# Performance work log

Measured on AMD Instinct MI355X. Metric: run time of the kernel, lower is better.

## Reference

```python
import jax, jax.numpy as jnp
import numpy as np

EPS = 1e-5   # BatchNorm eps
OUT = 256    # resize target


def _crop_bounds(img):
    # A row/col is 'whitespace' iff all its values are identical (len(unique)==1),
    # i.e. min == max along that axis. This fuses the torch while-loops into reductions.
    col_var = img.min(axis=0) != img.max(axis=0)   # [W] True where column non-constant
    row_var = img.min(axis=1) != img.max(axis=1)   # [H]
    H, W = img.shape
    any_c = jnp.any(col_var)
    any_r = jnp.any(row_var)
    left = jnp.where(any_c, jnp.argmax(col_var), 0)
    right = jnp.where(any_c, W - 1 - jnp.argmax(col_var[::-1]), W - 1)
    top = jnp.where(any_r, jnp.argmax(row_var), 0)
    bottom = jnp.where(any_r, H - 1 - jnp.argmax(row_var[::-1]), H - 1)
    return top, bottom, left, right


def _crop_resize_bilinear(img, top, bottom, left, right, out=OUT):
    # Fused crop + bilinear resize (align_corners=False, torchvision-style),
    # avoids data-dependent output shapes: sample 256x256 grid inside the crop box.
    def axis_coords(lo, hi):
        size = (hi - lo + 1).astype(jnp.float32)
        c = lo.astype(jnp.float32) + (jnp.arange(out, dtype=jnp.float32) + 0.5) * size / out - 0.5
        c0 = jnp.floor(c)
        w = c - c0
        i0 = jnp.clip(c0, lo, hi).astype(jnp.int32)
        i1 = jnp.clip(c0 + 1.0, lo, hi).astype(jnp.int32)
        return i0, i1, w
    y0, y1, wy = axis_coords(top, bottom)
    x0, x1, wx = axis_coords(left, right)
    g = lambda yi, xi: img[yi[:, None], xi[None, :]]   # [256,256] gather
    top_row = g(y0, x0) * (1.0 - wx)[None, :] + g(y0, x1) * wx[None, :]
    bot_row = g(y1, x0) * (1.0 - wx)[None, :] + g(y1, x1) * wx[None, :]
    return top_row * (1.0 - wy)[:, None] + bot_row * wy[:, None]


DN = ('NCHW', 'OIHW', 'NCHW')


def _conv_block(x, w, b, gamma, beta, mean, var):
    # l2l ConvBlock with max_pool=False: Conv2d(k=3, stride=2, pad=1) -> BN(eval) -> ReLU
    x = jax.lax.conv_general_dilated(x, w, (2, 2), [(1, 1), (1, 1)], dimension_numbers=DN)
    x = x + b[None, :, None, None]
    scale = gamma / jnp.sqrt(var + EPS)
    x = (x - mean[None, :, None, None]) * scale[None, :, None, None] + beta[None, :, None, None]
    return jax.nn.relu(x)


def _forward(image, conv0_w, conv0_b, convs_w, convs_b, bn_gamma, bn_beta, bn_mean, bn_var, head_w, head_b):
    t, b, l, r = _crop_bounds(image)
    resized = _crop_resize_bilinear(image, t, b, l, r)            # [256,256]
    im = (255.0 - resized)[None, None]                             # [1,1,256,256]
    ones_k = jnp.ones((1, 1, 3, 3), im.dtype)
    dil = jax.lax.conv_general_dilated(im, ones_k, (1, 1), 'SAME', rhs_dilation=(2, 2), dimension_numbers=DN)
    x = 255.0 - jnp.clip(dil, 0.0, 255.0)                          # [1,1,256,256]
    x = _conv_block(x, conv0_w, conv0_b, bn_gamma[0], bn_beta[0], bn_mean[0], bn_var[0])
    for i in range(4):  # fixed small layer count
        x = _conv_block(x, convs_w[i], convs_b[i], bn_gamma[i + 1], bn_beta[i + 1], bn_mean[i + 1], bn_var[i + 1])
    feat = x.mean(axis=(2, 3))                                     # [1,64]
    logits = feat @ head_w.T + head_b                              # [1,2]
    return logits


def setup_inputs() -> dict:
    key = jax.random.key(0)
    ks = jax.random.split(key, 12)
    H = W = 8192
    hidden, ways = 64, 2
    return {
        'image': jax.random.normal(ks[0], (H, W), dtype=jnp.float32),
        'conv0_w': jax.random.normal(ks[1], (hidden, 1, 3, 3), dtype=jnp.float32) * 0.1,
        'conv0_b': jax.random.normal(ks[2], (hidden,), dtype=jnp.float32) * 0.1,
        'convs_w': jax.random.normal(ks[3], (4, hidden, hidden, 3, 3), dtype=jnp.float32) * 0.05,
        'convs_b': jax.random.normal(ks[4], (4, hidden), dtype=jnp.float32) * 0.1,
        'bn_gamma': jnp.ones((5, hidden), dtype=jnp.float32) + 0.1 * jax.random.normal(ks[5], (5, hidden)),
        'bn_beta': jax.random.normal(ks[6], (5, hidden), dtype=jnp.float32) * 0.1,
        'bn_mean': jax.random.normal(ks[7], (5, hidden), dtype=jnp.float32) * 0.1,
        'bn_var': jax.random.uniform(ks[8], (5, hidden), dtype=jnp.float32, minval=0.5, maxval=1.5),
        'head_w': jax.random.normal(ks[9], (ways, hidden), dtype=jnp.float32) * 0.1,
        'head_b': jax.random.normal(ks[10], (ways,), dtype=jnp.float32) * 0.1,
    }


def reference(image, conv0_w, conv0_b, convs_w, convs_b, bn_gamma, bn_beta, bn_mean, bn_var, head_w, head_b):
    logits = _forward(image, conv0_w, conv0_b, convs_w, convs_b, bn_gamma, bn_beta, bn_mean, bn_var, head_w, head_b)
    return jnp.argmax(logits, axis=1)  # predicted_label, shape [1]
```

## Files before the change

### kernel.cpp

```cpp
#include <hip/hip_runtime.h>
#include <hip/hip_bf16.h>


#define IMG_H 8192
#define IMG_W 8192
#define EPS 1e-5f

__device__ __forceinline__ int scan_nonconst(const float* __restrict__ base,
                                             int n, long stride, int* sflag) {
  const int tid = threadIdx.x;
  const float ref = base[0];
  for (int start = 0; start < n; start += 1024) {
    if (tid == 0) *sflag = 0;
    __syncthreads();
    int f = 0;
#pragma unroll
    for (int u = 0; u < 4; ++u) {
      const int k = start + u * 256 + tid;
      if (k < n && base[(long)k * stride] != ref) f = 1;
    }
    if (f) *sflag = 1;
    __syncthreads();
    if (*sflag) return 1;
  }
  return 0;
}

__global__ __launch_bounds__(256) void crop_bounds_k(
    const float* __restrict__ img, int* __restrict__ bounds) {
  __shared__ int sflag;
  const int dir = blockIdx.x;
  if (dir == 0) {
    for (int r = 0; r < IMG_H; ++r)
      if (scan_nonconst(img + (long)r * IMG_W, IMG_W, 1, &sflag)) {
        if (threadIdx.x == 0) bounds[0] = r;
        return;
      }
    if (threadIdx.x == 0) bounds[0] = 0;
  } else if (dir == 1) {
    for (int r = IMG_H - 1; r >= 0; --r)
      if (scan_nonconst(img + (long)r * IMG_W, IMG_W, 1, &sflag)) {
        if (threadIdx.x == 0) bounds[1] = r;
        return;
      }
    if (threadIdx.x == 0) bounds[1] = IMG_H - 1;
  } else if (dir == 2) {
    for (int c = 0; c < IMG_W; ++c)
      if (scan_nonconst(img + c, IMG_H, IMG_W, &sflag)) {
        if (threadIdx.x == 0) bounds[2] = c;
        return;
      }
    if (threadIdx.x == 0) bounds[2] = 0;
  } else {
    for (int c = IMG_W - 1; c >= 0; --c)
      if (scan_nonconst(img + c, IMG_H, IMG_W, &sflag)) {
        if (threadIdx.x == 0) bounds[3] = c;
        return;
      }
    if (threadIdx.x == 0) bounds[3] = IMG_W - 1;
  }
}

__global__ __launch_bounds__(256) void resize_dilate_k(
    const float* __restrict__ img, const int* __restrict__ bounds,
    float* __restrict__ out) {
  __shared__ float s[3][256];
  const int i = blockIdx.x;
  const int j = threadIdx.x;
  const int tb = bounds[0], bb = bounds[1], lb = bounds[2], rb = bounds[3];
  const float sy = (float)(bb - tb + 1);
  const float sx = (float)(rb - lb + 1);

  const float cx = (float)lb + ((float)j + 0.5f) * sx / 256.0f - 0.5f;
  const float cx0 = floorf(cx);
  const float wx = cx - cx0;
  const int x0 = (int)fminf(fmaxf(cx0, (float)lb), (float)rb);
  const int x1 = (int)fminf(fmaxf(cx0 + 1.0f, (float)lb), (float)rb);

#pragma unroll
  for (int k = 0; k < 3; ++k) {
    const int row = i + 2 * (k - 1);
    float v = 0.0f;
    if ((unsigned)row < 256u) {
      const float cy = (float)tb + ((float)row + 0.5f) * sy / 256.0f - 0.5f;
      const float cy0 = floorf(cy);
      const float wy = cy - cy0;
      const int y0 = (int)fminf(fmaxf(cy0, (float)tb), (float)bb);
      const int y1 = (int)fminf(fmaxf(cy0 + 1.0f, (float)tb), (float)bb);
      const float v00 = img[(long)y0 * IMG_W + x0];
      const float v01 = img[(long)y0 * IMG_W + x1];
      const float v10 = img[(long)y1 * IMG_W + x0];
      const float v11 = img[(long)y1 * IMG_W + x1];
      const float tr = v00 * (1.0f - wx) + v01 * wx;
      const float br = v10 * (1.0f - wx) + v11 * wx;
      v = 255.0f - (tr * (1.0f - wy) + br * wy);
    }
    s[k][j] = v;
  }
  __syncthreads();

  float sum = 0.0f;
#pragma unroll
  for (int k = 0; k < 3; ++k) {
    const int y = i + 2 * (k - 1);
    if ((unsigned)y >= 256u) continue;
#pragma unroll
    for (int dx = -2; dx <= 2; dx += 2) {
      const int x = j + dx;
      if ((unsigned)x >= 256u) continue;
      sum += s[k][x];
    }
  }
  out[i * 256 + j] = 255.0f - fminf(fmaxf(sum, 0.0f), 255.0f);
}

template <int OCP>
__global__ __launch_bounds__(256) void conv_bn_relu_k(
    const float* __restrict__ in, const float* __restrict__ wt,
    const float* __restrict__ bias, const float* __restrict__ gamma,
    const float* __restrict__ beta, const float* __restrict__ mean,
    const float* __restrict__ var, float* __restrict__ out,
    int IC, int IH, int IW, int OH, int OW) {
  __shared__ float wl[OCP * 64 * 9];
  const int ocg = blockIdx.z * OCP;
  const int nW = OCP * IC * 9;
  for (int idx = threadIdx.x; idx < nW; idx += 256)
    wl[idx] = wt[(long)ocg * IC * 9 + idx];
  __syncthreads();

  const int ox = blockIdx.x * 16 + (threadIdx.x & 15);
  const int oy = blockIdx.y * 16 + (threadIdx.x >> 4);
  if (ox >= OW || oy >= OH) return;

  float acc[OCP];
#pragma unroll
  for (int o = 0; o < OCP; ++o) acc[o] = 0.0f;

  const int iy0 = 2 * oy - 1;
  const int ix0 = 2 * ox - 1;
  for (int ic = 0; ic < IC; ++ic) {
    const float* __restrict__ ip = in + (long)ic * IH * IW;
    const float* __restrict__ wp = wl + ic * 9;
#pragma unroll
    for (int ky = 0; ky < 3; ++ky) {
      const int iy = iy0 + ky;
      if ((unsigned)iy >= (unsigned)IH) continue;
#pragma unroll
      for (int kx = 0; kx < 3; ++kx) {
        const int ix = ix0 + kx;
        if ((unsigned)ix >= (unsigned)IW) continue;
        const float v = ip[(long)iy * IW + ix];
        const int t = ky * 3 + kx;
#pragma unroll
        for (int o = 0; o < OCP; ++o)
          acc[o] = fmaf(v, wp[o * IC * 9 + t], acc[o]);
      }
    }
  }

#pragma unroll
  for (int o = 0; o < OCP; ++o) {
    const int oc = ocg + o;
    const float s = gamma[oc] / sqrtf(var[oc] + EPS);
    const float v = (acc[o] + bias[oc] - mean[oc]) * s + beta[oc];
    out[((long)oc * OH + oy) * OW + ox] = fmaxf(v, 0.0f);
  }
}

__global__ __launch_bounds__(64) void conv4_k(
    const float* __restrict__ in, const float* __restrict__ wt,
    const float* __restrict__ bias, const float* __restrict__ gamma,
    const float* __restrict__ beta, const float* __restrict__ mean,
    const float* __restrict__ var, float* __restrict__ out) {
  __shared__ float wl[64 * 9];
  const int oc = blockIdx.x;
  for (int idx = threadIdx.x; idx < 576; idx += 64)
    wl[idx] = wt[oc * 576 + idx];
  __syncthreads();

  const int ox = threadIdx.x & 7;
  const int oy = threadIdx.x >> 3;
  const int iy0 = 2 * oy - 1;
  const int ix0 = 2 * ox - 1;
  float acc = 0.0f;
  for (int ic = 0; ic < 64; ++ic) {
    const float* __restrict__ ip = in + ic * 256;
    const float* __restrict__ wp = wl + ic * 9;
#pragma unroll
    for (int ky = 0; ky < 3; ++ky) {
      const int iy = iy0 + ky;
      if ((unsigned)iy >= 16u) continue;
#pragma unroll
      for (int kx = 0; kx < 3; ++kx) {
        const int ix = ix0 + kx;
        if ((unsigned)ix >= 16u) continue;
        acc = fmaf(ip[iy * 16 + ix], wp[ky * 3 + kx], acc);
      }
    }
  }
  const float s = gamma[oc] / sqrtf(var[oc] + EPS);
  const float v = (acc + bias[oc] - mean[oc]) * s + beta[oc];
  out[oc * 64 + threadIdx.x] = fmaxf(v, 0.0f);
}

__global__ __launch_bounds__(64) void head_argmax_k(
    const float* __restrict__ x, const float* __restrict__ hw,
    const float* __restrict__ hb, float* __restrict__ out) {
  const int c = threadIdx.x;
  float s = 0.0f;
#pragma unroll
  for (int k = 0; k < 64; ++k) s += x[c * 64 + k];
  const float feat = s * (1.0f / 64.0f);
  float p0 = feat * hw[c];
  float p1 = feat * hw[64 + c];
#pragma unroll
  for (int off = 32; off > 0; off >>= 1) {
    p0 += __shfl_down(p0, off);
    p1 += __shfl_down(p1, off);
  }
  if (c == 0) {
    const float l0 = p0 + hb[0];
    const float l1 = p1 + hb[1];
    out[0] = (l1 > l0) ? 1.0f : 0.0f;
  }
}

extern "C" void kernel_launch(void* const* d_in, const int* in_sizes, int n_in,
                              void* d_out, int out_size, void* d_ws,
                              size_t ws_size, hipStream_t stream) {
  const float* image   = (const float*)d_in[0];
  const float* conv0_w = (const float*)d_in[1];
  const float* conv0_b = (const float*)d_in[2];
  const float* convs_w = (const float*)d_in[3];
  const float* convs_b = (const float*)d_in[4];
  const float* bn_g    = (const float*)d_in[5];
  const float* bn_b    = (const float*)d_in[6];
  const float* bn_m    = (const float*)d_in[7];
  const float* bn_v    = (const float*)d_in[8];
  const float* head_w  = (const float*)d_in[9];
  const float* head_b  = (const float*)d_in[10];

  float* W = (float*)d_ws;
  int* bounds = (int*)d_ws;
  float* x1 = W + 16;
  float* c0 = x1 + 65536;
  float* c1 = c0 + 1048576;
  float* c2 = c1 + 262144;
  float* c3 = c2 + 65536;
  float* c4 = c3 + 16384;

  crop_bounds_k<<<4, 256, 0, stream>>>(image, bounds);
  resize_dilate_k<<<256, 256, 0, stream>>>(image, bounds, x1);

  conv_bn_relu_k<8><<<dim3(8, 8, 8), 256, 0, stream>>>(
      x1, conv0_w, conv0_b, bn_g, bn_b, bn_m, bn_v, c0, 1, 256, 256, 128, 128);
  conv_bn_relu_k<4><<<dim3(4, 4, 16), 256, 0, stream>>>(
      c0, convs_w + 0 * 36864, convs_b + 0 * 64, bn_g + 64, bn_b + 64,
      bn_m + 64, bn_v + 64, c1, 64, 128, 128, 64, 64);
  conv_bn_relu_k<2><<<dim3(2, 2, 32), 256, 0, stream>>>(
      c1, convs_w + 1 * 36864, convs_b + 1 * 64, bn_g + 128, bn_b + 128,
      bn_m + 128, bn_v + 128, c2, 64, 64, 64, 32, 32);
  conv_bn_relu_k<1><<<dim3(1, 1, 64), 256, 0, stream>>>(
      c2, convs_w + 2 * 36864, convs_b + 2 * 64, bn_g + 192, bn_b + 192,
      bn_m + 192, bn_v + 192, c3, 64, 32, 32, 16, 16);
  conv4_k<<<64, 64, 0, stream>>>(
      c3, convs_w + 3 * 36864, convs_b + 3 * 64, bn_g + 256, bn_b + 256,
      bn_m + 256, bn_v + 256, c4);

  head_argmax_k<<<1, 64, 0, stream>>>(c4, head_w, head_b, (float*)d_out);
}
```

Measured before the change: 629.8 us.

## Fuse tail conv layers and head into one persistent kernel with grid barriers

Replaces the last three conv launches and the head launch with one 256-block kernel that uses atomic-counter grid barriers between stages. It also splits input channels across blocks for conv3 and conv4, writing partial sums that a later stage reduces, so more blocks do useful work. The conv1 launch now uses fewer output channels per block to double its block count. The aim is to remove launch overhead and the under-occupied small-layer kernels. In exchange it adds spin-wait barriers, which rely on all 256 blocks being resident at once, plus extra partial-sum traffic.

Result: faster. 581.2 us (-7.7%).

```diff
diff --git a/kernel.cpp b/kernel.cpp
--- a/kernel.cpp
+++ b/kernel.cpp
@@ -27,8 +27,10 @@
 }
 
 __global__ __launch_bounds__(256) void crop_bounds_k(
-    const float* __restrict__ img, int* __restrict__ bounds) {
+    const float* __restrict__ img, int* __restrict__ bounds,
+    int* __restrict__ ctr) {
   __shared__ int sflag;
+  if (threadIdx.x == 0) ctr[0] = 0;
   const int dir = blockIdx.x;
   if (dir == 0) {
     for (int r = 0; r < IMG_H; ++r)
@@ -167,61 +169,167 @@
   }
 }
 
-__global__ __launch_bounds__(64) void conv4_k(
-    const float* __restrict__ in, const float* __restrict__ wt,
-    const float* __restrict__ bias, const float* __restrict__ gamma,
-    const float* __restrict__ beta, const float* __restrict__ mean,
-    const float* __restrict__ var, float* __restrict__ out) {
-  __shared__ float wl[64 * 9];
-  const int oc = blockIdx.x;
-  for (int idx = threadIdx.x; idx < 576; idx += 64)
-    wl[idx] = wt[oc * 576 + idx];
+__device__ __forceinline__ void gbar(int* ctr, int target) {
   __syncthreads();
-
-  const int ox = threadIdx.x & 7;
-  const int oy = threadIdx.x >> 3;
-  const int iy0 = 2 * oy - 1;
-  const int ix0 = 2 * ox - 1;
-  float acc = 0.0f;
-  for (int ic = 0; ic < 64; ++ic) {
-    const float* __restrict__ ip = in + ic * 256;
-    const float* __restrict__ wp = wl + ic * 9;
-#pragma unroll
-    for (int ky = 0; ky < 3; ++ky) {
-      const int iy = iy0 + ky;
-      if ((unsigned)iy >= 16u) continue;
-#pragma unroll
-      for (int kx = 0; kx < 3; ++kx) {
-        const int ix = ix0 + kx;
-        if ((unsigned)ix >= 16u) continue;
-        acc = fmaf(ip[iy * 16 + ix], wp[ky * 3 + kx], acc);
-      }
-    }
-  }
-  const float s = gamma[oc] / sqrtf(var[oc] + EPS);
-  const float v = (acc + bias[oc] - mean[oc]) * s + beta[oc];
-  out[oc * 64 + threadIdx.x] = fmaxf(v, 0.0f);
-}
-
-__global__ __launch_bounds__(64) void head_argmax_k(
-    const float* __restrict__ x, const float* __restrict__ hw,
-    const float* __restrict__ hb, float* __restrict__ out) {
-  const int c = threadIdx.x;
-  float s = 0.0f;
-#pragma unroll
-  for (int k = 0; k < 64; ++k) s += x[c * 64 + k];
-  const float feat = s * (1.0f / 64.0f);
-  float p0 = feat * hw[c];
-  float p1 = feat * hw[64 + c];
-#pragma unroll
-  for (int off = 32; off > 0; off >>= 1) {
-    p0 += __shfl_down(p0, off);
-    p1 += __shfl_down(p1, off);
-  }
-  if (c == 0) {
-    const float l0 = p0 + hb[0];
-    const float l1 = p1 + hb[1];
-    out[0] = (l1 > l0) ? 1.0f : 0.0f;
+  if (threadIdx.x == 0) {
+    __threadfence();
+    __hip_atomic_fetch_add(ctr, 1, __ATOMIC_RELEASE, __HIP_MEMORY_SCOPE_AGENT);
+    while (__hip_atomic_load(ctr, __ATOMIC_ACQUIRE,
+                             __HIP_MEMORY_SCOPE_AGENT) < target)
+      __builtin_amdgcn_s_sleep(1);
+  }
+  __syncthreads();
+}
+
+__global__ __launch_bounds__(256) void tail_fused_k(
+    const float* __restrict__ c1, const float* __restrict__ convs_w,
+    const float* __restrict__ convs_b, const float* __restrict__ bn_g,
+    const float* __restrict__ bn_b, const float* __restrict__ bn_m,
+    const float* __restrict__ bn_v, const float* __restrict__ head_w,
+    const float* __restrict__ head_b, float* __restrict__ c2,
+    float* __restrict__ c3, float* __restrict__ c4, float* __restrict__ p3,
+    float* __restrict__ p4, int* __restrict__ ctr, float* __restrict__ out) {
+  __shared__ float wl[576];
+  const int blk = blockIdx.x;
+  const int tid = threadIdx.x;
+
+  {
+    const int oc = blk >> 2;
+    const int pix = (blk & 3) * 256 + tid;
+    const float* wt = convs_w + 36864 + oc * 576;
+    for (int idx = tid; idx < 576; idx += 256) wl[idx] = wt[idx];
+    __syncthreads();
+    const int oy = pix >> 5, ox = pix & 31;
+    const int iy0 = 2 * oy - 1, ix0 = 2 * ox - 1;
+    float acc = 0.0f;
+    for (int ic = 0; ic < 64; ++ic) {
+      const float* __restrict__ ip = c1 + ic * 4096;
+      const float* __restrict__ wp = wl + ic * 9;
+#pragma unroll
+      for (int ky = 0; ky < 3; ++ky) {
+        const int iy = iy0 + ky;
+        if ((unsigned)iy >= 64u) continue;
+#pragma unroll
+        for (int kx = 0; kx < 3; ++kx) {
+          const int ix = ix0 + kx;
+          if ((unsigned)ix >= 64u) continue;
+          acc = fmaf(ip[iy * 64 + ix], wp[ky * 3 + kx], acc);
+        }
+      }
+    }
+    const float s = bn_g[128 + oc] / sqrtf(bn_v[128 + oc] + EPS);
+    c2[oc * 1024 + pix] =
+        fmaxf((acc + convs_b[64 + oc] - bn_m[128 + oc]) * s + bn_b[128 + oc],
+              0.0f);
+  }
+  gbar(ctr, 256);
+
+  {
+    const int icg = blk >> 6;
+    const int oc = blk & 63;
+    const float* wt = convs_w + 2 * 36864 + oc * 576 + icg * 144;
+    for (int idx = tid; idx < 144; idx += 256) wl[idx] = wt[idx];
+    __syncthreads();
+    const int oy = tid >> 4, ox = tid & 15;
+    const int iy0 = 2 * oy - 1, ix0 = 2 * ox - 1;
+    float acc = 0.0f;
+#pragma unroll 4
+    for (int i = 0; i < 16; ++i) {
+      const float* __restrict__ ip = c2 + (icg * 16 + i) * 1024;
+      const float* __restrict__ wp = wl + i * 9;
+#pragma unroll
+      for (int ky = 0; ky < 3; ++ky) {
+        const int iy = iy0 + ky;
+        if ((unsigned)iy >= 32u) continue;
+#pragma unroll
+        for (int kx = 0; kx < 3; ++kx) {
+          const int ix = ix0 + kx;
+          if ((unsigned)ix >= 32u) continue;
+          acc = fmaf(ip[iy * 32 + ix], wp[ky * 3 + kx], acc);
+        }
+      }
+    }
+    p3[blk * 256 + tid] = acc;
+  }
+  gbar(ctr, 512);
+
+  {
+    const int g = blk * 256 + tid;
+    if (g < 16384) {
+      const int oc = g >> 8;
+      const float v = p3[g] + p3[g + 16384] + p3[g + 32768] + p3[g + 49152];
+      const float s = bn_g[192 + oc] / sqrtf(bn_v[192 + oc] + EPS);
+      c3[g] = fmaxf(
+          (v + convs_b[128 + oc] - bn_m[192 + oc]) * s + bn_b[192 + oc], 0.0f);
+    }
+  }
+  gbar(ctr, 768);
+
+  {
+    const int icg = blk >> 4;
+    const int ocb = (blk & 15) * 4;
+    const float* wt = convs_w + 3 * 36864;
+    for (int idx = tid; idx < 144; idx += 256) {
+      const int o = idx / 36, r = idx % 36;
+      wl[idx] = wt[(ocb + o) * 576 + icg * 36 + r];
+    }
+    __syncthreads();
+    const int ol = tid >> 6;
+    const int pix = tid & 63;
+    const int oy = pix >> 3, ox = pix & 7;
+    const int iy0 = 2 * oy - 1, ix0 = 2 * ox - 1;
+    float acc = 0.0f;
+#pragma unroll
+    for (int i = 0; i < 4; ++i) {
+      const float* __restrict__ ip = c3 + (icg * 4 + i) * 256;
+      const float* __restrict__ wp = wl + ol * 36 + i * 9;
+#pragma unroll
+      for (int ky = 0; ky < 3; ++ky) {
+        const int iy = iy0 + ky;
+        if ((unsigned)iy >= 16u) continue;
+#pragma unroll
+        for (int kx = 0; kx < 3; ++kx) {
+          const int ix = ix0 + kx;
+          if ((unsigned)ix >= 16u) continue;
+          acc = fmaf(ip[iy * 16 + ix], wp[ky * 3 + kx], acc);
+        }
+      }
+    }
+    p4[blk * 256 + tid] = acc;
+  }
+  gbar(ctr, 1024);
+
+  {
+    const int g = blk * 256 + tid;
+    if (g < 4096) {
+      const int oc = g >> 6;
+      float v = 0.0f;
+#pragma unroll
+      for (int k = 0; k < 16; ++k) v += p4[g + k * 4096];
+      const float s = bn_g[256 + oc] / sqrtf(bn_v[256 + oc] + EPS);
+      c4[g] = fmaxf(
+          (v + convs_b[192 + oc] - bn_m[256 + oc]) * s + bn_b[256 + oc], 0.0f);
+    }
+  }
+  gbar(ctr, 1280);
+
+  if (blk == 0 && tid < 64) {
+    float ssum = 0.0f;
+#pragma unroll
+    for (int k = 0; k < 64; ++k) ssum += c4[tid * 64 + k];
+    const float feat = ssum * (1.0f / 64.0f);
+    float p0 = feat * head_w[tid];
+    float p1 = feat * head_w[64 + tid];
+#pragma unroll
+    for (int off = 32; off > 0; off >>= 1) {
+      p0 += __shfl_down(p0, off);
+      p1 += __shfl_down(p1, off);
+    }
+    if (tid == 0) {
+      const float l0 = p0 + head_b[0];
+      const float l1 = p1 + head_b[1];
+      out[0] = (l1 > l0) ? 1.0f : 0.0f;
+    }
   }
 }
 
@@ -242,30 +350,26 @@
 
   float* W = (float*)d_ws;
   int* bounds = (int*)d_ws;
+  int* ctr = (int*)d_ws + 8;
   float* x1 = W + 16;
   float* c0 = x1 + 65536;
   float* c1 = c0 + 1048576;
   float* c2 = c1 + 262144;
   float* c3 = c2 + 65536;
   float* c4 = c3 + 16384;
-
-  crop_bounds_k<<<4, 256, 0, stream>>>(image, bounds);
+  float* p3 = c4 + 4096;
+  float* p4 = p3 + 65536;
+
+  crop_bounds_k<<<4, 256, 0, stream>>>(image, bounds, ctr);
   resize_dilate_k<<<256, 256, 0, stream>>>(image, bounds, x1);
 
   conv_bn_relu_k<8><<<dim3(8, 8, 8), 256, 0, stream>>>(
       x1, conv0_w, conv0_b, bn_g, bn_b, bn_m, bn_v, c0, 1, 256, 256, 128, 128);
-  conv_bn_relu_k<4><<<dim3(4, 4, 16), 256, 0, stream>>>(
+  conv_bn_relu_k<2><<<dim3(4, 4, 32), 256, 0, stream>>>(
       c0, convs_w + 0 * 36864, convs_b + 0 * 64, bn_g + 64, bn_b + 64,
       bn_m + 64, bn_v + 64, c1, 64, 128, 128, 64, 64);
-  conv_bn_relu_k<2><<<dim3(2, 2, 32), 256, 0, stream>>>(
-      c1, convs_w + 1 * 36864, convs_b + 1 * 64, bn_g + 128, bn_b + 128,
-      bn_m + 128, bn_v + 128, c2, 64, 64, 64, 32, 32);
-  conv_bn_relu_k<1><<<dim3(1, 1, 64), 256, 0, stream>>>(
-      c2, convs_w + 2 * 36864, convs_b + 2 * 64, bn_g + 192, bn_b + 192,
-      bn_m + 192, bn_v + 192, c3, 64, 32, 32, 16, 16);
-  conv4_k<<<64, 64, 0, stream>>>(
-      c3, convs_w + 3 * 36864, convs_b + 3 * 64, bn_g + 256, bn_b + 256,
-      bn_m + 256, bn_v + 256, c4);
-
-  head_argmax_k<<<1, 64, 0, stream>>>(c4, head_w, head_b, (float*)d_out);
-}
+
+  tail_fused_k<<<256, 256, 0, stream>>>(
+      c1, convs_w, convs_b, bn_g, bn_b, bn_m, bn_v, head_w, head_b,
+      c2, c3, c4, p3, p4, ctr, (float*)d_out);
+}
```
